# Optimization experiments

Measured on AMD Instinct MI355X. Metric: run time of the kernel, lower is better.

Reference implementation:

```python
import jax, jax.numpy as jnp
import numpy as np

N_NODES = 50000
N_EDGES = 800000
IN_DIM, HID, OUT_DIM = 32, 96, 1
NEG_SLOPE = 0.2


def _glorot(key, shape):
    fan_in, fan_out = shape[0], shape[-1]
    lim = float(np.sqrt(6.0 / (fan_in + fan_out)))
    return jax.random.uniform(key, shape, jnp.float32, -lim, lim)


def setup_inputs() -> dict:
    key = jax.random.key(0)
    ks = jax.random.split(key, 20)
    inp = {
        "x": jax.random.normal(ks[0], (N_NODES, IN_DIM), jnp.float32),
        "edge_index": jax.random.randint(ks[1], (2, N_EDGES), 0, N_NODES, jnp.int64),
        "edge_weight": jax.random.uniform(ks[2], (N_EDGES,), jnp.float32),
    }
    dims = [(IN_DIM, HID), (HID, HID), (HID, HID), (HID, OUT_DIM)]
    names = ["0", "1", "2", "f"]
    k = 3
    for nm, (di, do) in zip(names, dims):
        inp["W" + nm] = _glorot(ks[k], (di, do)); k += 1
        inp["as" + nm] = _glorot(ks[k], (1, do))[0]; k += 1
        inp["ad" + nm] = _glorot(ks[k], (1, do))[0]; k += 1
        inp["b" + nm] = jnp.zeros((do,), jnp.float32)
    return inp


def _gat_conv(x, src, dst, n, W, a_s, a_d, b):
    # h: [N, out]; per-node attention logits, gathered per edge
    h = x @ W
    es = h @ a_s  # [N]
    ed = h @ a_d  # [N]
    e = jax.nn.leaky_relu(es[src] + ed[dst], NEG_SLOPE)  # [E]
    m = jax.ops.segment_max(e, dst, num_segments=n)  # segment-softmax (stable)
    ex = jnp.exp(e - m[dst])
    s = jax.ops.segment_sum(ex, dst, num_segments=n)
    alpha = ex / s[dst]  # every node has a self loop -> s > 0
    out = jax.ops.segment_sum(alpha[:, None] * h[src], dst, num_segments=n)
    return out + b


def reference(x, edge_index, edge_weight, W0, as0, ad0, b0, W1, as1, ad1, b1,
              W2, as2, ad2, b2, Wf, asf, adf, bf):
    # edge_weight is ignored: PyG GATConv with edge_dim=None drops edge_attr.
    n = x.shape[0]
    loops = jnp.arange(n, dtype=edge_index.dtype)
    src = jnp.concatenate([edge_index[0], loops])  # add_self_loops=True
    dst = jnp.concatenate([edge_index[1], loops])

    # dropout is identity in eval mode
    for (W, a_s, a_d, b) in [(W0, as0, ad0, b0), (W1, as1, ad1, b1), (W2, as2, ad2, b2)]:
        residual = x
        x = _gat_conv(x, src, dst, n, W, a_s, a_d, b)
        if x.shape == residual.shape:
            x = x + residual
        x = jax.nn.relu(x)
    return _gat_conv(x, src, dst, n, Wf, asf, adf, bf)
```

## Files before the change

kernel.cpp:

```cpp
#include <hip/hip_runtime.h>
#include <hip/hip_fp16.h>
#include <math.h>

#define N_NODES 50000
#define N_EDGES 800000
#define E_TOT   (N_EDGES + N_NODES)
#define IN_DIM  32
#define HID     96
#define NEG_SLOPE 0.2f
#define BUCKET  48
#define G_PAD   50
#define FILL_EPT 4
#define FILL_NB ((E_TOT + 256 * FILL_EPT - 1) / (256 * FILL_EPT))
#define AGG_BLOCKS (N_NODES / 16)
#define PREP_BLOCKS ((N_NODES * 32) / 256)
#define WT_BLOCKS (((HID * HID) + 255) / 256)

typedef _Float16 half8v __attribute__((ext_vector_type(8)));
typedef float    float4v __attribute__((ext_vector_type(4)));

static inline int cdiv(long long a, int b) { return (int)((a + b - 1) / b); }

__device__ __forceinline__ int clamp_src(int s) {
    return (int)min((unsigned)s, (unsigned)(N_NODES - 1));
}

__global__ __launch_bounds__(256) void build_prep_kernel(
    const int* __restrict__ ei, unsigned* __restrict__ cnt,
    unsigned short* __restrict__ srcs,
    const float* __restrict__ x, const float* __restrict__ W0,
    const float* __restrict__ as0, const float* __restrict__ ad0,
    __half* __restrict__ xh, float* __restrict__ es, float* __restrict__ ed,
    const float* __restrict__ W1, const float* __restrict__ W2,
    __half* __restrict__ WT1, __half* __restrict__ WT2) {
    int b = blockIdx.x;
    if (b < FILL_NB) {
        int e0 = (b * 256 + threadIdx.x) * FILL_EPT;
        if (e0 >= E_TOT) return;
        if (e0 < N_EDGES) {
            int4 d4 = *(const int4*)(ei + N_EDGES + e0);
            int4 s4 = *(const int4*)(ei + e0);
            int dd[4] = {d4.x, d4.y, d4.z, d4.w};
            int ss[4] = {s4.x, s4.y, s4.z, s4.w};
            #pragma unroll
            for (int k = 0; k < 4; ++k) {
                int d = clamp_src(dd[k]);
                unsigned pos = atomicAdd(cnt + d, 1u);
                if (pos < BUCKET) srcs[(size_t)d * BUCKET + pos] = (unsigned short)clamp_src(ss[k]);
            }
        } else {
            #pragma unroll
            for (int k = 0; k < 4; ++k) {
                int d = e0 + k - N_EDGES;
                unsigned pos = atomicAdd(cnt + d, 1u);
                if (pos < BUCKET) srcs[(size_t)d * BUCKET + pos] = (unsigned short)d;
            }
        }
        return;
    }
    b -= FILL_NB;
    if (b >= PREP_BLOCKS) {
        int i = (b - PREP_BLOCKS) * 256 + threadIdx.x;
        if (i < HID * HID) {
            int n = i / HID, k = i - n * HID;
            WT1[i] = __float2half(W1[k * HID + n]);
            WT2[i] = __float2half(W2[k * HID + n]);
        }
        return;
    }
    __shared__ float s_us[32], s_ud[32];
    if (threadIdx.x < 64) {
        int k = threadIdx.x & 31;
        int sel = threadIdx.x >> 5;
        const float* a = sel ? ad0 : as0;
        float acc = 0.f;
        #pragma unroll 8
        for (int c = 0; c < HID; ++c) acc += W0[k * HID + c] * a[c];
        if (sel) s_ud[k] = acc; else s_us[k] = acc;
    }
    __syncthreads();
    int idx = b * 256 + threadIdx.x;
    int node = idx >> 5;
    int k = threadIdx.x & 31;
    float xv = x[(size_t)node * 32 + k];
    float xnb = __shfl_xor(xv, 1);
    if ((k & 1) == 0) {
        __half2 h2v = __floats2half2_rn(xv, xnb);
        ((__half2*)xh)[((size_t)node * 32 + k) >> 1] = h2v;
    }
    float ps = xv * s_us[k], pd = xv * s_ud[k];
    #pragma unroll
    for (int o = 16; o; o >>= 1) {
        ps += __shfl_xor(ps, o);
        pd += __shfl_xor(pd, o);
    }
    if (k == 0) { es[node] = ps; ed[node] = pd; }
}

__global__ __launch_bounds__(256) void aggregate32_kernel(
    const unsigned* __restrict__ cnt, const unsigned short* __restrict__ srcs,
    const float* __restrict__ es, const float* __restrict__ ed,
    const __half* __restrict__ xh, float* __restrict__ agg) {
    __shared__ uint2 sh[4][4][G_PAD];
    int lane = threadIdx.x & 63;
    int wv = threadIdx.x >> 6;
    int g = lane >> 4, lin = lane & 15;
    int node = blockIdx.x * 16 + wv * 4 + g;
    size_t row = (size_t)node * BUCKET;
    int deg = min((int)cnt[node], BUCKET);
    float edv = ed[node];

    float lsum = 0.f;
    float4 acc = {0.f, 0.f, 0.f, 0.f};
    const uint2* x2 = (const uint2*)xh;
    int h8sel = lin >> 3;
    int c = lin & 7;

    for (int j = lin; j < deg; j += 16) {
        int s = clamp_src(srcs[row + j]);
        float v = es[s] + edv;
        v = v > 0.f ? v : NEG_SLOPE * v;
        float e = __expf(v);
        uint2 p; p.x = (unsigned)s; p.y = __float_as_uint(e);
        sh[wv][g][j] = p;
        lsum += e;
    }
    int j = 0;
    for (; j + 4 <= deg; j += 4) {
        uint2 p0 = sh[wv][g][j + h8sel];
        uint2 p1 = sh[wv][g][j + 2 + h8sel];
        uint2 q0 = x2[(size_t)p0.x * 8 + c];
        uint2 q1 = x2[(size_t)p1.x * 8 + c];
        float e0 = __uint_as_float(p0.y), e1 = __uint_as_float(p1.y);
        float2 f00 = __half22float2(*(__half2*)&q0.x);
        float2 f01 = __half22float2(*(__half2*)&q0.y);
        float2 f10 = __half22float2(*(__half2*)&q1.x);
        float2 f11 = __half22float2(*(__half2*)&q1.y);
        acc.x += e0 * f00.x + e1 * f10.x; acc.y += e0 * f00.y + e1 * f10.y;
        acc.z += e0 * f01.x + e1 * f11.x; acc.w += e0 * f01.y + e1 * f11.y;
    }
    for (; j < deg; j += 2) {
        int idx = j + h8sel;
        if (idx < deg) {
            uint2 p = sh[wv][g][idx];
            uint2 q = x2[(size_t)p.x * 8 + c];
            float e = __uint_as_float(p.y);
            float2 f0 = __half22float2(*(__half2*)&q.x);
            float2 f1 = __half22float2(*(__half2*)&q.y);
            acc.x += e * f0.x; acc.y += e * f0.y;
            acc.z += e * f1.x; acc.w += e * f1.y;
        }
    }
    #pragma unroll
    for (int o = 1; o < 16; o <<= 1) lsum += __shfl_xor(lsum, o);
    acc.x += __shfl_xor(acc.x, 8);
    acc.y += __shfl_xor(acc.y, 8);
    acc.z += __shfl_xor(acc.z, 8);
    acc.w += __shfl_xor(acc.w, 8);
    if (lin < 8) {
        float inv = 1.f / lsum;
        float4 o4; o4.x = acc.x * inv; o4.y = acc.y * inv; o4.z = acc.z * inv; o4.w = acc.w * inv;
        ((float4*)agg)[(size_t)node * 8 + lin] = o4;
    }
}

__global__ void gemm32_kernel(const float* __restrict__ agg, const float* __restrict__ W,
                              const float* __restrict__ b, __half* __restrict__ out16) {
    int idx = blockIdx.x * blockDim.x + threadIdx.x;
    if (idx >= (N_NODES / 4) * 24) return;
    int g   = idx / 24;
    int c4q = idx - g * 24;
    int n0 = g * 4;
    const float4* Xa = (const float4*)agg + (size_t)n0 * 8;
    const float4* Xb = Xa + 8;
    const float4* Xc = Xb + 8;
    const float4* Xd = Xc + 8;
    const float4* W4 = (const float4*)W;

    float4 accA = {0,0,0,0}, accB = {0,0,0,0}, accC = {0,0,0,0}, accD = {0,0,0,0};
    for (int k4 = 0; k4 < 8; ++k4) {
        float4 xa = Xa[k4], xb = Xb[k4], xc = Xc[k4], xd = Xd[k4];
        #pragma unroll
        for (int kk = 0; kk < 4; ++kk) {
            float4 w = W4[(size_t)(k4 * 4 + kk) * 24 + c4q];
            float sa = ((const float*)&xa)[kk], sb = ((const float*)&xb)[kk];
            float sc = ((const float*)&xc)[kk], sd = ((const float*)&xd)[kk];
            accA.x += sa * w.x; accA.y += sa * w.y; accA.z += sa * w.z; accA.w += sa * w.w;
            accB.x += sb * w.x; accB.y += sb * w.y; accB.z += sb * w.z; accB.w += sb * w.w;
            accC.x += sc * w.x; accC.y += sc * w.y; accC.z += sc * w.z; accC.w += sc * w.w;
            accD.x += sd * w.x; accD.y += sd * w.y; accD.z += sd * w.z; accD.w += sd * w.w;
        }
    }
    float4 bb = ((const float4*)b)[c4q];
    uint2* O16 = (uint2*)out16;
    #pragma unroll
    for (int nn = 0; nn < 4; ++nn) {
        float4 a = (nn == 0) ? accA : (nn == 1) ? accB : (nn == 2) ? accC : accD;
        float rx = fmaxf(a.x + bb.x, 0.f), ry = fmaxf(a.y + bb.y, 0.f);
        float rz = fmaxf(a.z + bb.z, 0.f), rw = fmaxf(a.w + bb.w, 0.f);
        __half2 q0 = __floats2half2_rn(rx, ry), q1 = __floats2half2_rn(rz, rw);
        uint2 st; st.x = *(unsigned*)&q0; st.y = *(unsigned*)&q1;
        O16[(size_t)(n0 + nn) * 24 + c4q] = st;
    }
}

__global__ __launch_bounds__(256) void mfma_gemm96_kernel(
    const __half* __restrict__ x16, const __half* __restrict__ wt,
    const float* __restrict__ a_s, const float* __restrict__ a_d,
    __half* __restrict__ h, float* __restrict__ es, float* __restrict__ ed) {
    __shared__ __align__(16) __half s_t[4][16][104];
    int wid = (int)((blockIdx.x * 256 + threadIdx.x) >> 6);
    if (wid >= N_NODES / 16) return;
    int lane = threadIdx.x & 63;
    int wvl = threadIdx.x >> 6;
    int col = lane & 15, quad = lane >> 4;
    int m0 = wid * 16;
    const __half* arow = x16 + (size_t)(m0 + col) * 96 + quad * 8;
    const __half* brow = wt + (size_t)col * 96 + quad * 8;

    float4v acc[6];
    #pragma unroll
    for (int t = 0; t < 6; ++t) acc[t] = (float4v){0.f, 0.f, 0.f, 0.f};

    #pragma unroll
    for (int ks = 0; ks < 3; ++ks) {
        half8v afrag = *(const half8v*)(arow + ks * 32);
        #pragma unroll
        for (int t = 0; t < 6; ++t) {
            half8v bfrag = *(const half8v*)(brow + (size_t)t * 16 * 96 + ks * 32);
            acc[t] = __builtin_amdgcn_mfma_f32_16x16x32_f16(afrag, bfrag, acc[t], 0, 0, 0);
        }
    }

    float ps0 = 0.f, ps1 = 0.f, ps2 = 0.f, ps3 = 0.f;
    float pd0 = 0.f, pd1 = 0.f, pd2 = 0.f, pd3 = 0.f;
    #pragma unroll
    for (int t = 0; t < 6; ++t) {
        int ch = t * 16 + col;
        float sa = a_s[ch], sd = a_d[ch];
        float v0 = acc[t][0], v1 = acc[t][1], v2 = acc[t][2], v3 = acc[t][3];
        int r0 = quad * 4;
        s_t[wvl][r0 + 0][ch] = __float2half(v0);
        s_t[wvl][r0 + 1][ch] = __float2half(v1);
        s_t[wvl][r0 + 2][ch] = __float2half(v2);
        s_t[wvl][r0 + 3][ch] = __float2half(v3);
        ps0 += v0 * sa; ps1 += v1 * sa; ps2 += v2 * sa; ps3 += v3 * sa;
        pd0 += v0 * sd; pd1 += v1 * sd; pd2 += v2 * sd; pd3 += v3 * sd;
    }
    #pragma unroll
    for (int o = 1; o < 16; o <<= 1) {
        ps0 += __shfl_xor(ps0, o); ps1 += __shfl_xor(ps1, o);
        ps2 += __shfl_xor(ps2, o); ps3 += __shfl_xor(ps3, o);
        pd0 += __shfl_xor(pd0, o); pd1 += __shfl_xor(pd1, o);
        pd2 += __shfl_xor(pd2, o); pd3 += __shfl_xor(pd3, o);
    }
    if (col == 0) {
        int nb = m0 + quad * 4;
        es[nb] = ps0; es[nb + 1] = ps1; es[nb + 2] = ps2; es[nb + 3] = ps3;
        ed[nb] = pd0; ed[nb + 1] = pd1; ed[nb + 2] = pd2; ed[nb + 3] = pd3;
    }
    {
        int trow = lane >> 2, q = lane & 3;
        const uint4* sr = (const uint4*)&s_t[wvl][trow][0];
        uint4* H8 = (uint4*)h;
        size_t rb = (size_t)(m0 + trow) * 12;
        H8[rb + q]     = sr[q];
        H8[rb + q + 4] = sr[q + 4];
        H8[rb + q + 8] = sr[q + 8];
    }
}

__global__ __launch_bounds__(256) void aggregate96_kernel(
    const unsigned* __restrict__ cnt, const unsigned short* __restrict__ srcs,
    const float* __restrict__ es, const float* __restrict__ ed,
    const __half* __restrict__ h, const float* __restrict__ b,
    const __half* __restrict__ res16, __half* __restrict__ out16,
    const float* __restrict__ Wf, float* __restrict__ hfin, int do_relu) {
    __shared__ uint2 sh[4][4][G_PAD];
    int lane = threadIdx.x & 63;
    int wv = threadIdx.x >> 6;
    int g = lane >> 4, lin = lane & 15;
    int node = blockIdx.x * 16 + wv * 4 + g;
    size_t row = (size_t)node * BUCKET;
    int deg = min((int)cnt[node], BUCKET);
    float edv = ed[node];

    float lsum = 0.f;
    float a0 = 0.f, a1 = 0.f, a2 = 0.f, a3 = 0.f, a4 = 0.f, a5 = 0.f, a6 = 0.f, a7 = 0.f;
    const uint4* h8 = (const uint4*)h;
    bool act = (lin < 12);

    for (int j = lin; j < deg; j += 16) {
        int s = clamp_src(srcs[row + j]);
        float v = es[s] + edv;
        v = v > 0.f ? v : NEG_SLOPE * v;
        float e = __expf(v);
        uint2 p; p.x = (unsigned)s; p.y = __float_as_uint(e);
        sh[wv][g][j] = p;
        lsum += e;
    }
    int j = 0;
    for (; j + 2 <= deg; j += 2) {
        uint2 p0 = sh[wv][g][j];
        uint2 p1 = sh[wv][g][j + 1];
        if (act) {
            uint4 q0 = h8[(size_t)p0.x * 12 + lin];
            uint4 q1 = h8[(size_t)p1.x * 12 + lin];
            float e0 = __uint_as_float(p0.y), e1 = __uint_as_float(p1.y);
            float2 fa0 = __half22float2(*(__half2*)&q0.x);
            float2 fa1 = __half22float2(*(__half2*)&q0.y);
            float2 fa2 = __half22float2(*(__half2*)&q0.z);
            float2 fa3 = __half22float2(*(__half2*)&q0.w);
            float2 fb0 = __half22float2(*(__half2*)&q1.x);
            float2 fb1 = __half22float2(*(__half2*)&q1.y);
            float2 fb2 = __half22float2(*(__half2*)&q1.z);
            float2 fb3 = __half22float2(*(__half2*)&q1.w);
            a0 += e0 * fa0.x + e1 * fb0.x; a1 += e0 * fa0.y + e1 * fb0.y;
            a2 += e0 * fa1.x + e1 * fb1.x; a3 += e0 * fa1.y + e1 * fb1.y;
            a4 += e0 * fa2.x + e1 * fb2.x; a5 += e0 * fa2.y + e1 * fb2.y;
            a6 += e0 * fa3.x + e1 * fb3.x; a7 += e0 * fa3.y + e1 * fb3.y;
        }
    }
    if (j < deg) {
        uint2 p = sh[wv][g][j];
        if (act) {
            uint4 q = h8[(size_t)p.x * 12 + lin];
            float e = __uint_as_float(p.y);
            float2 f0 = __half22float2(*(__half2*)&q.x);
            float2 f1 = __half22float2(*(__half2*)&q.y);
            float2 f2 = __half22float2(*(__half2*)&q.z);
            float2 f3 = __half22float2(*(__half2*)&q.w);
            a0 += e * f0.x; a1 += e * f0.y;
            a2 += e * f1.x; a3 += e * f1.y;
            a4 += e * f2.x; a5 += e * f2.y;
            a6 += e * f3.x; a7 += e * f3.y;
        }
    }
    #pragma unroll
    for (int o = 1; o < 16; o <<= 1) lsum += __shfl_xor(lsum, o);

    float pfin = 0.f;
    if (act) {
        float inv = 1.f / lsum;
        const float4* b4 = (const float4*)b;
        float4 bb0 = b4[lin * 2], bb1 = b4[lin * 2 + 1];
        float v0 = a0 * inv + bb0.x, v1 = a1 * inv + bb0.y;
        float v2 = a2 * inv + bb0.z, v3 = a3 * inv + bb0.w;
        float v4 = a4 * inv + bb1.x, v5 = a5 * inv + bb1.y;
        float v6 = a6 * inv + bb1.z, v7 = a7 * inv + bb1.w;
        if (res16) {
            uint4 rr = ((const uint4*)res16)[(size_t)node * 12 + lin];
            float2 r0 = __half22float2(*(__half2*)&rr.x);
            float2 r1 = __half22float2(*(__half2*)&rr.y);
            float2 r2 = __half22float2(*(__half2*)&rr.z);
            float2 r3 = __half22float2(*(__half2*)&rr.w);
            v0 += r0.x; v1 += r0.y; v2 += r1.x; v3 += r1.y;
            v4 += r2.x; v5 += r2.y; v6 += r3.x; v7 += r3.y;
        }
        if (do_relu) {
            v0 = fmaxf(v0, 0.f); v1 = fmaxf(v1, 0.f); v2 = fmaxf(v2, 0.f); v3 = fmaxf(v3, 0.f);
            v4 = fmaxf(v4, 0.f); v5 = fmaxf(v5, 0.f); v6 = fmaxf(v6, 0.f); v7 = fmaxf(v7, 0.f);
        }
        if (out16) {
            __half2 q0 = __floats2half2_rn(v0, v1), q1 = __floats2half2_rn(v2, v3);
            __half2 q2 = __floats2half2_rn(v4, v5), q3 = __floats2half2_rn(v6, v7);
            uint4 st; st.x = *(unsigned*)&q0; st.y = *(unsigned*)&q1;
            st.z = *(unsigned*)&q2; st.w = *(unsigned*)&q3;
            ((uint4*)out16)[(size_t)node * 12 + lin] = st;
        }
        if (hfin) {
            const float4* w4 = (const float4*)Wf;
            float4 wf0 = w4[lin * 2], wf1 = w4[lin * 2 + 1];
            pfin = v0 * wf0.x + v1 * wf0.y + v2 * wf0.z + v3 * wf0.w
                 + v4 * wf1.x + v5 * wf1.y + v6 * wf1.z + v7 * wf1.w;
        }
    }
    if (hfin) {
        #pragma unroll
        for (int o = 1; o < 16; o <<= 1) pfin += __shfl_xor(pfin, o);
        if (lin == 0) hfin[node] = pfin;
    }
}

__global__ __launch_bounds__(256) void aggregate1_kernel(
    const unsigned* __restrict__ cnt, const unsigned short* __restrict__ srcs,
    const float* __restrict__ hfin, const float* __restrict__ asf,
    const float* __restrict__ adf, const float* __restrict__ bf,
    float* __restrict__ out) {
    int lane = threadIdx.x & 63;
    int wv = threadIdx.x >> 6;
    int g = lane >> 4, lin = lane & 15;
    int node = blockIdx.x * 16 + wv * 4 + g;
    size_t row = (size_t)node * BUCKET;
    int deg = min((int)cnt[node], BUCKET);
    float as0 = asf[0], ad0 = adf[0];
    float edv = hfin[node] * ad0;

    float lsum = 0.f, acc = 0.f;
    for (int j = lin; j < deg; j += 16) {
        int s = clamp_src(srcs[row + j]);
        float hs = hfin[s];
        float v = as0 * hs + edv;
        v = v > 0.f ? v : NEG_SLOPE * v;
        float ex = __expf(v);
        lsum += ex;
        acc += ex * hs;
    }
    #pragma unroll
    for (int o = 1; o < 16; o <<= 1) {
        lsum += __shfl_xor(lsum, o);
        acc  += __shfl_xor(acc, o);
    }
    if (lin == 0) out[node] = acc / lsum + bf[0];
}


extern "C" void kernel_launch(void* const* d_in, const int* in_sizes, int n_in,
                              void* d_out, int out_size, void* d_ws, size_t ws_size,
                              hipStream_t stream) {
    const float* x  = (const float*)d_in[0];
    const int*   ei = (const int*)d_in[1];
    const float* W0 = (const float*)d_in[3];
    const float* as0 = (const float*)d_in[4];
    const float* ad0 = (const float*)d_in[5];
    const float* b0 = (const float*)d_in[6];
    const float* W1 = (const float*)d_in[7];
    const float* as1 = (const float*)d_in[8];
    const float* ad1 = (const float*)d_in[9];
    const float* b1 = (const float*)d_in[10];
    const float* W2 = (const float*)d_in[11];
    const float* as2 = (const float*)d_in[12];
    const float* ad2 = (const float*)d_in[13];
    const float* b2 = (const float*)d_in[14];
    const float* Wf = (const float*)d_in[15];
    const float* asf = (const float*)d_in[16];
    const float* adf = (const float*)d_in[17];
    const float* bf = (const float*)d_in[18];

    float* out = (float*)d_out;

    float* Hf = (float*)d_ws;
    __half* H16 = (__half*)Hf;
    float* ES = Hf + (long long)N_NODES * HID;
    float* ED = ES + N_NODES;
    unsigned* CNT = (unsigned*)(ED + N_NODES);
    unsigned short* SRCS = (unsigned short*)(CNT + N_NODES);
    __half* X16A = (__half*)(SRCS + (size_t)N_NODES * BUCKET);
    __half* X16B = X16A + (size_t)N_NODES * HID;
    __half* WT1 = X16B + (size_t)N_NODES * HID;
    __half* WT2 = WT1 + HID * HID;
    float* HFIN = (float*)(WT2 + HID * HID);
    __half* XH = (__half*)(HFIN + N_NODES);
    float* AGG = (float*)Hf;

    hipMemsetAsync(CNT, 0, (size_t)N_NODES * sizeof(unsigned), stream);
    build_prep_kernel<<<FILL_NB + PREP_BLOCKS + WT_BLOCKS, 256, 0, stream>>>(
        ei, CNT, SRCS, x, W0, as0, ad0, XH, ES, ED, W1, W2, WT1, WT2);

    const int gemm_threads = (N_NODES / 4) * 24;
    const int mfma_blocks = cdiv(N_NODES / 16, 4);

    aggregate32_kernel<<<AGG_BLOCKS, 256, 0, stream>>>(CNT, SRCS, ES, ED, XH, AGG);
    gemm32_kernel<<<cdiv(gemm_threads, 256), 256, 0, stream>>>(AGG, W0, b0, X16A);

    mfma_gemm96_kernel<<<mfma_blocks, 256, 0, stream>>>(X16A, WT1, as1, ad1, H16, ES, ED);
    aggregate96_kernel<<<AGG_BLOCKS, 256, 0, stream>>>(
        CNT, SRCS, ES, ED, H16, b1, X16A, X16B, nullptr, nullptr, 1);

    mfma_gemm96_kernel<<<mfma_blocks, 256, 0, stream>>>(X16B, WT2, as2, ad2, H16, ES, ED);
    aggregate96_kernel<<<AGG_BLOCKS, 256, 0, stream>>>(
        CNT, SRCS, ES, ED, H16, b2, X16B, nullptr, Wf, HFIN, 1);

    aggregate1_kernel<<<AGG_BLOCKS, 256, 0, stream>>>(CNT, SRCS, HFIN, asf, adf, bf, out);
}
```

Baseline: 278.6 us.

## Build per-node source buckets via two-level binning with shared-memory atomics

Replaces direct global atomics on per-node counters with a two-pass scheme. The first pass bins edges into 196 coarse bins of 256 destination nodes using shared-memory ranks and one global atomic per bin per block. A new kernel then builds each node's source list in shared memory and writes it out coalesced, inserting the self loop first. The aim is to cut contended scattered global atomics and scattered 2-byte writes, at the cost of an extra kernel launch and an intermediate edge buffer whose fixed per-bin capacity (5120) could overflow on skewed graphs.

```diff
diff --git a/kernel.cpp b/kernel.cpp
--- a/kernel.cpp
+++ b/kernel.cpp
@@ -10,8 +10,10 @@
 #define NEG_SLOPE 0.2f
 #define BUCKET  48
 #define G_PAD   50
+#define NBINS   196
+#define BCAP    5120
 #define FILL_EPT 4
-#define FILL_NB ((E_TOT + 256 * FILL_EPT - 1) / (256 * FILL_EPT))
+#define FILL_NB ((N_EDGES + 256 * FILL_EPT - 1) / (256 * FILL_EPT))
 #define AGG_BLOCKS (N_NODES / 16)
 #define PREP_BLOCKS ((N_NODES * 32) / 256)
 #define WT_BLOCKS (((HID * HID) + 255) / 256)
@@ -26,8 +28,8 @@
 }
 
 __global__ __launch_bounds__(256) void build_prep_kernel(
-    const int* __restrict__ ei, unsigned* __restrict__ cnt,
-    unsigned short* __restrict__ srcs,
+    const int* __restrict__ ei, unsigned* __restrict__ gcnt,
+    unsigned* __restrict__ ebuf,
     const float* __restrict__ x, const float* __restrict__ W0,
     const float* __restrict__ as0, const float* __restrict__ ad0,
     __half* __restrict__ xh, float* __restrict__ es, float* __restrict__ ed,
@@ -35,25 +37,38 @@
     __half* __restrict__ WT1, __half* __restrict__ WT2) {
     int b = blockIdx.x;
     if (b < FILL_NB) {
-        int e0 = (b * 256 + threadIdx.x) * FILL_EPT;
-        if (e0 >= E_TOT) return;
-        if (e0 < N_EDGES) {
+        __shared__ unsigned lcnt[256];
+        __shared__ unsigned lbase[256];
+        int tid = threadIdx.x;
+        lcnt[tid] = 0u;
+        __syncthreads();
+        int e0 = (b * 256 + tid) * FILL_EPT;
+        bool val = e0 < N_EDGES;
+        int binv[FILL_EPT]; unsigned rank[FILL_EPT], pk[FILL_EPT];
+        if (val) {
             int4 d4 = *(const int4*)(ei + N_EDGES + e0);
             int4 s4 = *(const int4*)(ei + e0);
             int dd[4] = {d4.x, d4.y, d4.z, d4.w};
             int ss[4] = {s4.x, s4.y, s4.z, s4.w};
             #pragma unroll
-            for (int k = 0; k < 4; ++k) {
+            for (int k = 0; k < FILL_EPT; ++k) {
                 int d = clamp_src(dd[k]);
-                unsigned pos = atomicAdd(cnt + d, 1u);
-                if (pos < BUCKET) srcs[(size_t)d * BUCKET + pos] = (unsigned short)clamp_src(ss[k]);
+                binv[k] = d >> 8;
+                pk[k] = (unsigned)clamp_src(ss[k]) | ((unsigned)(d & 255) << 16);
+                rank[k] = atomicAdd(&lcnt[binv[k]], 1u);
             }
-        } else {
+        }
+        __syncthreads();
+        if (tid < NBINS) {
+            unsigned c = lcnt[tid];
+            lbase[tid] = c ? atomicAdd(gcnt + tid, c) : 0u;
+        }
+        __syncthreads();
+        if (val) {
             #pragma unroll
-            for (int k = 0; k < 4; ++k) {
-                int d = e0 + k - N_EDGES;
-                unsigned pos = atomicAdd(cnt + d, 1u);
-                if (pos < BUCKET) srcs[(size_t)d * BUCKET + pos] = (unsigned short)d;
+            for (int k = 0; k < FILL_EPT; ++k) {
+                unsigned pos = lbase[binv[k]] + rank[k];
+                if (pos < BCAP) ebuf[(size_t)binv[k] * BCAP + pos] = pk[k];
             }
         }
         return;
@@ -95,6 +110,33 @@
         pd += __shfl_xor(pd, o);
     }
     if (k == 0) { es[node] = ps; ed[node] = pd; }
+}
+
+__global__ __launch_bounds__(256) void bucket_build_kernel(
+    const unsigned* __restrict__ gcnt, const unsigned* __restrict__ ebuf,
+    unsigned* __restrict__ cnt, unsigned short* __restrict__ srcs) {
+    __shared__ unsigned short lsr[256][BUCKET];
+    __shared__ unsigned lct[256];
+    int bin = blockIdx.x, tid = threadIdx.x;
+    int nb = bin * 256 + tid;
+    lct[tid] = 1u;
+    lsr[tid][0] = (unsigned short)min(nb, N_NODES - 1);
+    __syncthreads();
+    unsigned ec = min(gcnt[bin], (unsigned)BCAP);
+    for (unsigned j = tid; j < ec; j += 256) {
+        unsigned pkv = ebuf[(size_t)bin * BCAP + j];
+        unsigned dloc = (pkv >> 16) & 255u;
+        unsigned pos = atomicAdd(&lct[dloc], 1u);
+        if (pos < BUCKET) lsr[dloc][pos] = (unsigned short)(pkv & 0xFFFFu);
+    }
+    __syncthreads();
+    if (nb < N_NODES) cnt[nb] = min(lct[tid], (unsigned)BUCKET);
+    const uint4* ls4 = (const uint4*)&lsr[0][0];
+    uint4* gs4 = (uint4*)(srcs + (size_t)bin * 256 * BUCKET);
+    for (int i = tid; i < 256 * (BUCKET / 8); i += 256) {
+        int node = i / (BUCKET / 8);
+        if (bin * 256 + node < N_NODES) gs4[i] = ls4[i];
+    }
 }
 
 __global__ __launch_bounds__(256) void aggregate32_kernel(
@@ -451,11 +493,14 @@
     __half* WT2 = WT1 + HID * HID;
     float* HFIN = (float*)(WT2 + HID * HID);
     __half* XH = (__half*)(HFIN + N_NODES);
+    unsigned* GCNT = (unsigned*)(XH + (size_t)N_NODES * 32);
+    unsigned* EBUF = GCNT + NBINS;
     float* AGG = (float*)Hf;
 
-    hipMemsetAsync(CNT, 0, (size_t)N_NODES * sizeof(unsigned), stream);
+    hipMemsetAsync(GCNT, 0, (size_t)NBINS * sizeof(unsigned), stream);
     build_prep_kernel<<<FILL_NB + PREP_BLOCKS + WT_BLOCKS, 256, 0, stream>>>(
-        ei, CNT, SRCS, x, W0, as0, ad0, XH, ES, ED, W1, W2, WT1, WT2);
+        ei, GCNT, EBUF, x, W0, as0, ad0, XH, ES, ED, W1, W2, WT1, WT2);
+    bucket_build_kernel<<<NBINS, 256, 0, stream>>>(GCNT, EBUF, CNT, SRCS);
 
     const int gemm_threads = (N_NODES / 4) * 24;
     const int mfma_blocks = cdiv(N_NODES / 16, 4);
```

After: 264.9 us. 1.05x faster.
